# Kernel optimization log

Hardware: AMD Instinct MI355X
Metric: run time of the kernel (lower is better)

## Reference

```python
import jax, jax.numpy as jnp
import numpy as np

EPS = 1e-07


def setup_inputs() -> dict:
    key = jax.random.key(0)
    k1, k2, k3 = jax.random.split(key, 3)
    B, C, H, W, K = 4, 64, 512, 512, 19
    x = jax.random.normal(k1, (B, C, H, W), dtype=jnp.float32)
    gt = jax.random.randint(k2, (B, H, W), 0, K, dtype=jnp.int32)
    aug_rand_info = jax.random.uniform(k3, (B, K, K), dtype=jnp.float32)
    return {"x": x, "gt": gt, "aug_rand_info": aug_rand_info}


def reference(x, gt, aug_rand_info):
    # x: [B,C,H,W], gt: [B,H,W] int labels in [0,K), aug_rand_info: [B,K,K]
    B, C, H, W = x.shape
    K = aug_rand_info.shape[1]
    HW = H * W
    # global segment id = b*K + class
    seg = (jnp.arange(B, dtype=jnp.int32)[:, None] * K + gt.reshape(B, HW)).reshape(-1)
    xf = x.reshape(B, C, HW).transpose(0, 2, 1).reshape(B * HW, C)  # [B*HW, C]
    # per-(image,class) sums and counts (segment reduce)
    sums = jax.ops.segment_sum(xf, seg, num_segments=B * K).reshape(B, K, C)
    cnt = jax.ops.segment_sum(jnp.ones((B * HW,), x.dtype), seg, num_segments=B * K).reshape(B, K, 1)
    valid = cnt > 0
    cnt_safe = jnp.where(valid, cnt, jnp.ones_like(cnt))
    mean = sums / cnt_safe                                     # [B,K,C]
    mean_px = mean.reshape(B * K, C)[seg]                      # gather per pixel
    var = jax.ops.segment_sum((xf - mean_px) ** 2, seg, num_segments=B * K).reshape(B, K, C) / cnt_safe
    std = jnp.sqrt(var) + EPS                                  # [B,K,C]
    # Dirichlet-style mixing weights over classes present in each image
    validf = valid.astype(x.dtype).reshape(B, 1, K)            # [B,1,K]
    w = aug_rand_info * validf                                 # zero out absent source classes
    w = w / jnp.clip(w.sum(-1, keepdims=True), EPS)            # renormalize -> simplex
    mix_mean = jnp.einsum('bck,bkd->bcd', w, mean)             # [B,K,C] style mean per target class
    mix_std = jnp.einsum('bck,bkd->bcd', w, std)
    # fused gather + per-class normalize + style scatter (class masks are disjoint)
    idx = gt.reshape(B, HW)[:, :, None]                        # [B,HW,1]
    take = lambda t: jnp.take_along_axis(t, idx, axis=1)       # [B,HW,C]
    m, s = take(mean), take(std)
    mm, ms = take(mix_mean), take(mix_std)
    xn = (xf.reshape(B, HW, C) - m) / s * ms + mm
    x_style = xn.transpose(0, 2, 1).reshape(B, C, H, W)
    return x_style
```

## Files before the change

kernel.cpp:

```cpp
#include <hip/hip_runtime.h>

#define EPSF 1e-7f

constexpr int Bn = 4, Cn = 64, Kn = 19;
constexpr int HWn = 512 * 512;

constexpr int SCH   = 128;
constexpr int SPIX  = HWn / SCH;
constexpr int SBLK  = 512;
constexpr int TSTR  = 2056;
constexpr int PARTSZ = 2464;

typedef float f32x16_t __attribute__((ext_vector_type(16)));
typedef float f32x4_t  __attribute__((ext_vector_type(4)));
typedef short bf16x8_t __attribute__((ext_vector_type(8)));

#define PKBF(lo, hi) ((__builtin_bit_cast(unsigned, (hi)) & 0xFFFF0000u) | \
                      (__builtin_bit_cast(unsigned, (lo)) >> 16))

__global__ __launch_bounds__(SBLK, 4) void k_stats(
    const float* __restrict__ x, const int* __restrict__ gt,
    float* __restrict__ part)
{
    __shared__ unsigned short tile[16 * TSTR];
    __shared__ int   lab[SPIX];
    __shared__ float credL[32];

    const int tid  = threadIdx.x;
    const int lane = tid & 63;
    const int w    = tid >> 6;
    const int g    = lane >> 5;
    const int col  = lane & 31;
    const int ch16 = col & 15;

    const int b    = blockIdx.x >> 7;
    const int pix0 = (blockIdx.x & 127) * SPIX;
    const float* xb  = x  + (size_t)b * Cn * HWn + pix0;
    const int*   gtb = gt + (size_t)b * HWn + pix0;

    {
        const int4 v = *reinterpret_cast<const int4*>(gtb + tid * 4);
        int4 cl;
        cl.x = min(max(v.x, 0), Kn - 1); cl.y = min(max(v.y, 0), Kn - 1);
        cl.z = min(max(v.z, 0), Kn - 1); cl.w = min(max(v.w, 0), Kn - 1);
        *reinterpret_cast<int4*>(&lab[tid * 4]) = cl;
    }

    f32x16_t dR0 = (f32x16_t)0.f, dR1 = (f32x16_t)0.f;
    f32x16_t dR2 = (f32x16_t)0.f, dR3 = (f32x16_t)0.f;
    int cnt = 0;

#define STAGE_(R) { \
    _Pragma("unroll") \
    for (int cc = 0; cc < 2; ++cc) { \
        const float* src = xb + (size_t)((R) * 16 + w * 2 + cc) * HWn; \
        unsigned short* dst = &tile[(w * 2 + cc) * TSTR]; \
        _Pragma("unroll") \
        for (int i = 0; i < 8; ++i) { \
            const float4 v = *reinterpret_cast<const float4*>(src + i * 256 + lane * 4); \
            uint2 pk; pk.x = PKBF(v.x, v.y); pk.y = PKBF(v.z, v.w); \
            *reinterpret_cast<uint2*>(&dst[i * 256 + lane * 4]) = pk; \
        } \
    } }

#define COMPUTE_(R, D, CNTON) { \
    _Pragma("unroll 1") \
    for (int s = 0; s < 16; ++s) { \
        const int pg = w * 256 + s * 16 + 8 * g; \
        uint4 bw = *reinterpret_cast<const uint4*>(&tile[ch16 * TSTR + pg]); \
        if (col >= 16) { \
            const float f0 = __builtin_bit_cast(float, bw.x << 16); \
            const float f1 = __builtin_bit_cast(float, bw.x & 0xFFFF0000u); \
            const float f2 = __builtin_bit_cast(float, bw.y << 16); \
            const float f3 = __builtin_bit_cast(float, bw.y & 0xFFFF0000u); \
            const float f4 = __builtin_bit_cast(float, bw.z << 16); \
            const float f5 = __builtin_bit_cast(float, bw.z & 0xFFFF0000u); \
            const float f6 = __builtin_bit_cast(float, bw.w << 16); \
            const float f7 = __builtin_bit_cast(float, bw.w & 0xFFFF0000u); \
            bw.x = PKBF(f0 * f0, f1 * f1); bw.y = PKBF(f2 * f2, f3 * f3); \
            bw.z = PKBF(f4 * f4, f5 * f5); bw.w = PKBF(f6 * f6, f7 * f7); \
        } \
        const int4 L0 = *reinterpret_cast<const int4*>(&lab[pg]); \
        const int4 L1 = *reinterpret_cast<const int4*>(&lab[pg + 4]); \
        const bool e0 = (L0.x == col), e1 = (L0.y == col); \
        const bool e2 = (L0.z == col), e3 = (L0.w == col); \
        const bool e4 = (L1.x == col), e5 = (L1.y == col); \
        const bool e6 = (L1.z == col), e7 = (L1.w == col); \
        int4 av; \
        av.x = (e0 ? 0x3F80u : 0u) | (e1 ? 0x3F800000u : 0u); \
        av.y = (e2 ? 0x3F80u : 0u) | (e3 ? 0x3F800000u : 0u); \
        av.z = (e4 ? 0x3F80u : 0u) | (e5 ? 0x3F800000u : 0u); \
        av.w = (e6 ? 0x3F80u : 0u) | (e7 ? 0x3F800000u : 0u); \
        if (CNTON) cnt += (int)e0 + (int)e1 + (int)e2 + (int)e3 \
                        + (int)e4 + (int)e5 + (int)e6 + (int)e7; \
        D = __builtin_amdgcn_mfma_f32_32x32x16_bf16( \
                __builtin_bit_cast(bf16x8_t, av), \
                __builtin_bit_cast(bf16x8_t, bw), D, 0, 0, 0); \
    } }

    __syncthreads();
    STAGE_(0)
    __syncthreads();
    COMPUTE_(0, dR0, true)
    __syncthreads();
    STAGE_(1)
    __syncthreads();
    COMPUTE_(1, dR1, false)
    __syncthreads();
    STAGE_(2)
    __syncthreads();
    COMPUTE_(2, dR2, false)
    __syncthreads();
    STAGE_(3)
    __syncthreads();
    COMPUTE_(3, dR3, false)

    const int cnt2 = cnt + __shfl(cnt, col + 32, 64);

    __syncthreads();
    float* redf = reinterpret_cast<float*>(tile);
    const int statO = (col >> 4) * 64;
#define RED_(R, D, OP) { \
    _Pragma("unroll") \
    for (int r = 0; r < 16; ++r) { \
        const int krow = (r & 3) + 8 * (r >> 2) + 4 * g; \
        if (krow < Kn) redf[krow * 128 + statO + (R) * 16 + ch16] OP D[r]; \
    } }
    #pragma unroll 1
    for (int ww = 0; ww < 8; ++ww) {
        if (w == ww) {
            if (ww == 0) { RED_(0, dR0, =)  RED_(1, dR1, =)  RED_(2, dR2, =)  RED_(3, dR3, =) }
            else         { RED_(0, dR0, +=) RED_(1, dR1, +=) RED_(2, dR2, +=) RED_(3, dR3, +=) }
            if (lane < Kn) {
                if (ww == 0) credL[lane]  = (float)cnt2;
                else         credL[lane] += (float)cnt2;
            }
        }
        __syncthreads();
    }

    float* pb = part + (size_t)blockIdx.x * PARTSZ;
    for (int i = tid; i < 2 * Cn * Kn; i += SBLK) {
        const int stat = i / (Cn * Kn);
        const int rr   = i - stat * (Cn * Kn);
        const int c = rr / Kn, k = rr - c * Kn;
        pb[i] = redf[k * 128 + stat * 64 + c];
    }
    if (tid < Kn) pb[2 * Cn * Kn + tid] = credL[tid];
}

__global__ __launch_bounds__(1024) void k_tables(
    const float* __restrict__ part, const float* __restrict__ aug,
    float* __restrict__ tabAB)
{
    __shared__ float mean_s[Kn * Cn];
    __shared__ float std_s [Kn * Cn];
    __shared__ float wrow  [Kn * Kn];
    __shared__ float wsum  [Kn];
    __shared__ float validf[Kn], cntf[Kn];

    const int b = blockIdx.x, tid = threadIdx.x;
    const float* pbase = part + (size_t)b * SCH * PARTSZ;

    if (tid < Kn) {
        float s = 0.f;
        for (int blk = 0; blk < SCH; ++blk)
            s += pbase[(size_t)blk * PARTSZ + 2 * Cn * Kn + tid];
        validf[tid] = (s > 0.f) ? 1.f : 0.f;
        cntf[tid]   = (s > 0.f) ? s : 1.f;
    }
    __syncthreads();

    for (int i = tid; i < Cn * Kn; i += 1024) {
        float s = 0.f, q = 0.f;
        for (int blk = 0; blk < SCH; ++blk) {
            s += pbase[(size_t)blk * PARTSZ + i];
            q += pbase[(size_t)blk * PARTSZ + Cn * Kn + i];
        }
        const int c = i / Kn, k = i - c * Kn;
        const float cs  = cntf[k];
        const float m   = s / cs;
        const float var = fmaxf(q / cs - m * m, 0.f);
        mean_s[k * Cn + c] = m;
        std_s [k * Cn + c] = sqrtf(var) + EPSF;
    }
    for (int i = tid; i < Kn * Kn; i += 1024) {
        const int t = i / Kn, k = i - t * Kn;
        wrow[i] = aug[((size_t)b * Kn + t) * Kn + k] * validf[k];
    }
    __syncthreads();
    if (tid < Kn) {
        float s = 0.f;
        for (int k = 0; k < Kn; ++k) s += wrow[tid * Kn + k];
        wsum[tid] = fmaxf(s, EPSF);
    }
    __syncthreads();
    for (int i = tid; i < Kn * Cn; i += 1024) {
        const int t = i >> 6, c = i & 63;
        const float inv = 1.f / wsum[t];
        float mm = 0.f, ms = 0.f;
        for (int k = 0; k < Kn; ++k) {
            const float wk = wrow[t * Kn + k] * inv;
            mm += wk * mean_s[k * Cn + c];
            ms += wk * std_s [k * Cn + c];
        }
        const float A  = ms / std_s[t * Cn + c];
        const float Bv = mm - mean_s[t * Cn + c] * A;
        const size_t o = ((size_t)b * Cn * Kn + c * Kn + t) * 2;
        tabAB[o + 0] = A;
        tabAB[o + 1] = Bv;
    }
}

constexpr int ABLK = 1024;
constexpr int ACH  = 64;
constexpr int APIX = HWn / ACH;

__global__ __launch_bounds__(ABLK, 4) void k_apply(
    const float* __restrict__ x, const int* __restrict__ gt,
    const float* __restrict__ tabAB, float* __restrict__ out)
{
    __shared__ float ABs[Cn * Kn * 2];
    const int tid   = threadIdx.x;
    const int b     = blockIdx.x >> 6;
    const int chunk = blockIdx.x & 63;

    for (int i = tid; i < Cn * Kn * 2; i += ABLK)
        ABs[i] = tabAB[(size_t)b * Cn * Kn * 2 + i];
    __syncthreads();

    const int p0 = chunk * APIX + tid * 4;
    const int4 L = *reinterpret_cast<const int4*>(gt + (size_t)b * HWn + p0);
    const int l0 = min(max(L.x, 0), Kn - 1);
    const int l1 = min(max(L.y, 0), Kn - 1);
    const int l2 = min(max(L.z, 0), Kn - 1);
    const int l3 = min(max(L.w, 0), Kn - 1);

    const float* xp = x   + (size_t)b * Cn * HWn + p0;
    float*       op = out + (size_t)b * Cn * HWn + p0;

    #pragma unroll 4
    for (int c = 0; c < Cn; ++c) {
        const float4 v = *reinterpret_cast<const float4*>(xp + (size_t)c * HWn);
        const int co = c * Kn;
        const float2 ab0 = *reinterpret_cast<const float2*>(&ABs[(co + l0) * 2]);
        const float2 ab1 = *reinterpret_cast<const float2*>(&ABs[(co + l1) * 2]);
        const float2 ab2 = *reinterpret_cast<const float2*>(&ABs[(co + l2) * 2]);
        const float2 ab3 = *reinterpret_cast<const float2*>(&ABs[(co + l3) * 2]);
        float4 o;
        o.x = v.x * ab0.x + ab0.y;
        o.y = v.y * ab1.x + ab1.y;
        o.z = v.z * ab2.x + ab2.y;
        o.w = v.w * ab3.x + ab3.y;
        __builtin_nontemporal_store(__builtin_bit_cast(f32x4_t, o),
                                    reinterpret_cast<f32x4_t*>(op + (size_t)c * HWn));
    }
}

extern "C" void kernel_launch(void* const* d_in, const int* in_sizes, int n_in,
                              void* d_out, int out_size, void* d_ws, size_t ws_size,
                              hipStream_t stream) {
    const float* x   = (const float*)d_in[0];
    const int*   gt  = (const int*)d_in[1];
    const float* aug = (const float*)d_in[2];
    float* out = (float*)d_out;

    float* part  = (float*)d_ws;
    float* tabAB = part + (size_t)Bn * SCH * PARTSZ;

    k_stats <<<dim3(Bn * SCH), dim3(SBLK), 0, stream>>>(x, gt, part);
    k_tables<<<dim3(Bn),       dim3(1024), 0, stream>>>(part, aug, tabAB);
    k_apply <<<dim3(Bn * ACH), dim3(ABLK), 0, stream>>>(x, gt, tabAB, out);
}
```

Measured before the change: 174.5 us.

## Stage stats tiles via direct global-to-LDS loads in fp32, split pixels into two phases

The stats kernel now copies x into shared memory with global_load_lds (direct global-to-LDS DMA) instead of loading through registers and packing to bf16. The tile holds fp32, so each pass covers half the pixels, and the schedule becomes 8 rounds (4 channel groups by 2 pixel halves). The bf16 conversion and squaring move into the compute loop. This removes the VGPR round trip and packing from staging, at the cost of more barriers and rounds, plus the same count of per-element converts now done at compute time.

```diff
diff --git a/kernel.cpp b/kernel.cpp
--- a/kernel.cpp
+++ b/kernel.cpp
@@ -8,7 +8,7 @@
 constexpr int SCH   = 128;
 constexpr int SPIX  = HWn / SCH;
 constexpr int SBLK  = 512;
-constexpr int TSTR  = 2056;
+constexpr int TSTR4 = 1028;
 constexpr int PARTSZ = 2464;
 
 typedef float f32x16_t __attribute__((ext_vector_type(16)));
@@ -17,12 +17,19 @@
 
 #define PKBF(lo, hi) ((__builtin_bit_cast(unsigned, (hi)) & 0xFFFF0000u) | \
                       (__builtin_bit_cast(unsigned, (lo)) >> 16))
+
+typedef const __attribute__((address_space(1))) void gas_void;
+typedef __attribute__((address_space(3))) void las_void;
+
+__device__ __forceinline__ void gload16(const float* g, float* l) {
+    __builtin_amdgcn_global_load_lds((gas_void*)g, (las_void*)l, 16, 0, 0);
+}
 
 __global__ __launch_bounds__(SBLK, 4) void k_stats(
     const float* __restrict__ x, const int* __restrict__ gt,
     float* __restrict__ part)
 {
-    __shared__ unsigned short tile[16 * TSTR];
+    __shared__ float tile[16 * TSTR4];
     __shared__ int   lab[SPIX];
     __shared__ float credL[32];
 
@@ -46,42 +53,36 @@
         *reinterpret_cast<int4*>(&lab[tid * 4]) = cl;
     }
 
-    f32x16_t dR0 = (f32x16_t)0.f, dR1 = (f32x16_t)0.f;
-    f32x16_t dR2 = (f32x16_t)0.f, dR3 = (f32x16_t)0.f;
+    f32x16_t dG0 = (f32x16_t)0.f, dG1 = (f32x16_t)0.f;
+    f32x16_t dG2 = (f32x16_t)0.f, dG3 = (f32x16_t)0.f;
     int cnt = 0;
 
-#define STAGE_(R) { \
+#define STAGE_(CG, PH) { \
     _Pragma("unroll") \
     for (int cc = 0; cc < 2; ++cc) { \
-        const float* src = xb + (size_t)((R) * 16 + w * 2 + cc) * HWn; \
-        unsigned short* dst = &tile[(w * 2 + cc) * TSTR]; \
+        const int row = w * 2 + cc; \
+        const float* src = xb + (size_t)((CG) * 16 + row) * HWn + (PH) * 1024 + lane * 4; \
+        float* dst = &tile[row * TSTR4]; \
         _Pragma("unroll") \
-        for (int i = 0; i < 8; ++i) { \
-            const float4 v = *reinterpret_cast<const float4*>(src + i * 256 + lane * 4); \
-            uint2 pk; pk.x = PKBF(v.x, v.y); pk.y = PKBF(v.z, v.w); \
-            *reinterpret_cast<uint2*>(&dst[i * 256 + lane * 4]) = pk; \
-        } \
+        for (int seg = 0; seg < 4; ++seg) \
+            gload16(src + seg * 256, dst + seg * 256); \
     } }
 
-#define COMPUTE_(R, D, CNTON) { \
+#define COMPUTE_(PH, D, CNTON) { \
     _Pragma("unroll 1") \
-    for (int s = 0; s < 16; ++s) { \
-        const int pg = w * 256 + s * 16 + 8 * g; \
-        uint4 bw = *reinterpret_cast<const uint4*>(&tile[ch16 * TSTR + pg]); \
-        if (col >= 16) { \
-            const float f0 = __builtin_bit_cast(float, bw.x << 16); \
-            const float f1 = __builtin_bit_cast(float, bw.x & 0xFFFF0000u); \
-            const float f2 = __builtin_bit_cast(float, bw.y << 16); \
-            const float f3 = __builtin_bit_cast(float, bw.y & 0xFFFF0000u); \
-            const float f4 = __builtin_bit_cast(float, bw.z << 16); \
-            const float f5 = __builtin_bit_cast(float, bw.z & 0xFFFF0000u); \
-            const float f6 = __builtin_bit_cast(float, bw.w << 16); \
-            const float f7 = __builtin_bit_cast(float, bw.w & 0xFFFF0000u); \
-            bw.x = PKBF(f0 * f0, f1 * f1); bw.y = PKBF(f2 * f2, f3 * f3); \
-            bw.z = PKBF(f4 * f4, f5 * f5); bw.w = PKBF(f6 * f6, f7 * f7); \
-        } \
-        const int4 L0 = *reinterpret_cast<const int4*>(&lab[pg]); \
-        const int4 L1 = *reinterpret_cast<const int4*>(&lab[pg + 4]); \
+    for (int s = 0; s < 8; ++s) { \
+        const int pg = w * 128 + s * 16 + 8 * g; \
+        const float4 va = *reinterpret_cast<const float4*>(&tile[ch16 * TSTR4 + pg]); \
+        const float4 vb = *reinterpret_cast<const float4*>(&tile[ch16 * TSTR4 + pg + 4]); \
+        float v0 = va.x, v1 = va.y, v2 = va.z, v3 = va.w; \
+        float v4 = vb.x, v5 = vb.y, v6 = vb.z, v7 = vb.w; \
+        if (col >= 16) { v0 *= v0; v1 *= v1; v2 *= v2; v3 *= v3; \
+                         v4 *= v4; v5 *= v5; v6 *= v6; v7 *= v7; } \
+        uint4 bw; \
+        bw.x = PKBF(v0, v1); bw.y = PKBF(v2, v3); \
+        bw.z = PKBF(v4, v5); bw.w = PKBF(v6, v7); \
+        const int4 L0 = *reinterpret_cast<const int4*>(&lab[(PH) * 1024 + pg]); \
+        const int4 L1 = *reinterpret_cast<const int4*>(&lab[(PH) * 1024 + pg + 4]); \
         const bool e0 = (L0.x == col), e1 = (L0.y == col); \
         const bool e2 = (L0.z == col), e3 = (L0.w == col); \
         const bool e4 = (L1.x == col), e5 = (L1.y == col); \
@@ -98,27 +99,24 @@
                 __builtin_bit_cast(bf16x8_t, bw), D, 0, 0, 0); \
     } }
 
-    __syncthreads();
-    STAGE_(0)
-    __syncthreads();
-    COMPUTE_(0, dR0, true)
-    __syncthreads();
-    STAGE_(1)
-    __syncthreads();
-    COMPUTE_(1, dR1, false)
-    __syncthreads();
-    STAGE_(2)
-    __syncthreads();
-    COMPUTE_(2, dR2, false)
-    __syncthreads();
-    STAGE_(3)
-    __syncthreads();
-    COMPUTE_(3, dR3, false)
+#define ROUND_(CG, PH, D, CNTON) \
+    STAGE_(CG, PH) \
+    __syncthreads(); \
+    COMPUTE_(PH, D, CNTON) \
+    __syncthreads();
+
+    ROUND_(0, 0, dG0, true)
+    ROUND_(1, 0, dG1, false)
+    ROUND_(2, 0, dG2, false)
+    ROUND_(3, 0, dG3, false)
+    ROUND_(0, 1, dG0, true)
+    ROUND_(1, 1, dG1, false)
+    ROUND_(2, 1, dG2, false)
+    ROUND_(3, 1, dG3, false)
 
     const int cnt2 = cnt + __shfl(cnt, col + 32, 64);
 
-    __syncthreads();
-    float* redf = reinterpret_cast<float*>(tile);
+    float* redf = tile;
     const int statO = (col >> 4) * 64;
 #define RED_(R, D, OP) { \
     _Pragma("unroll") \
@@ -129,8 +127,8 @@
     #pragma unroll 1
     for (int ww = 0; ww < 8; ++ww) {
         if (w == ww) {
-            if (ww == 0) { RED_(0, dR0, =)  RED_(1, dR1, =)  RED_(2, dR2, =)  RED_(3, dR3, =) }
-            else         { RED_(0, dR0, +=) RED_(1, dR1, +=) RED_(2, dR2, +=) RED_(3, dR3, +=) }
+            if (ww == 0) { RED_(0, dG0, =)  RED_(1, dG1, =)  RED_(2, dG2, =)  RED_(3, dG3, =) }
+            else         { RED_(0, dG0, +=) RED_(1, dG1, +=) RED_(2, dG2, +=) RED_(3, dG3, +=) }
             if (lane < Kn) {
                 if (ww == 0) credL[lane]  = (float)cnt2;
                 else         credL[lane] += (float)cnt2;
```

New measurement: 174.5 us. Within noise of the previous version (-0.0%).
